# Performance work log

Measured on AMD Instinct MI355X. Metric: run time of the kernel, lower is better.

The kernel has to match this reference:

```python
import jax, jax.numpy as jnp
import numpy as np

# Module config (matches init_kwargs)
SHAPE = (96, 128, 128)   # (D, H, W)
NUM_LAYERS = 2
K, S, P, DIL = 3, 2, 1, 1  # kernel, stride, padding, dilation (dilation=1)


def _sparse_maxpool(feat, mask):
    """One SparseMaxPool3d layer on a densified sparse tensor.

    feat: [B, D, H, W, C] float, inactive sites hold dtype-min
    mask: [B, D, H, W, 1] float 0/1 activity mask
    Max is taken only over ACTIVE input sites in each window (spconv semantics);
    an output site is active iff any input in its window is active.
    """
    neg = jnp.finfo(feat.dtype).min
    window = (1, K, K, K, 1)
    strides = (1, S, S, S, 1)
    pad = [(0, 0), (P, P), (P, P), (P, P), (0, 0)]
    masked = jnp.where(mask > 0, feat, neg)
    pooled = jax.lax.reduce_window(masked, neg, jax.lax.max, window, strides, pad)
    mask_out = jax.lax.reduce_window(mask, jnp.array(0, feat.dtype).item() * 0.0,
                                     jax.lax.max, window, strides, pad)
    return pooled, mask_out


def setup_inputs() -> dict:
    key = jax.random.key(0)
    k1, k2, k3, k4, k5 = jax.random.split(key, 5)
    N, C, B = 200000, 32, 2
    D, H, W = SHAPE
    features = jax.random.normal(k1, (N, C), dtype=jnp.float32)
    b = jax.random.randint(k2, (N,), 0, B)
    z = jax.random.randint(k3, (N,), 0, D)
    y = jax.random.randint(k4, (N,), 0, H)
    x = jax.random.randint(k5, (N,), 0, W)
    coors = jnp.stack([b, z, y, x], axis=1).astype(jnp.int32)
    return {"features": features, "coors": coors, "batch_size": B}


def reference(features, coors, batch_size):
    D, H, W = SHAPE
    C = features.shape[1]
    b, z, y, x = coors[:, 0], coors[:, 1], coors[:, 2], coors[:, 3]
    neg = jnp.finfo(features.dtype).min
    # Densify the sparse tensor (duplicate coords resolved by max, inactive = -inf)
    dense = jnp.full((batch_size, D, H, W, C), neg, features.dtype)
    dense = dense.at[b, z, y, x].max(features)
    mask = jnp.zeros((batch_size, D, H, W, 1), features.dtype).at[b, z, y, x].set(1.0)
    for _ in range(NUM_LAYERS):
        dense, mask = _sparse_maxpool(dense, mask)
    # Equivalent of SparseConvTensor.dense(): inactive output sites are 0
    return jnp.where(mask > 0, dense, jnp.zeros((), features.dtype))
```

## Files before the change

### kernel.cpp

```cpp
#include <hip/hip_runtime.h>
#include <cfloat>
#include <cstdint>

#define B_    2
#define OD    24
#define OH    32
#define OW    32
#define NC    32
#define NBINS (B_ * OD * OH * OW)
#define RSTRIDE 16
#define OVF_CAP 100000

#define TZ 4
#define TY 4
#define TX 4
#define TCELLS 64
#define NTZ (OD/TZ)
#define NTY (OH/TY)
#define NTX (OW/TX)
#define NTILES (B_*NTZ*NTY*NTX)
#define NBZ (TZ+1)
#define NBY (TY+1)
#define NBX (TX+1)
#define NB  (NBZ*NBY*NBX)
#define LIST_CAP 1792

__device__ __forceinline__ unsigned xform(float f) {
    unsigned u = __float_as_uint(f);
    return u ^ ((unsigned)((int)u >> 31) | 0x80000000u);
}
__device__ __forceinline__ float unxform(unsigned t) {
    return (t == 0u) ? 0.0f
           : __uint_as_float((t >> 31) ? (t ^ 0x80000000u) : ~t);
}

__device__ __forceinline__ void slow_apply(unsigned* sm_out, const float* feat,
                                           int rec, int fm, int cb) {
    unsigned idx = ((unsigned)rec) >> 8;
    for (int c2 = 0; c2 < NC; ++c2) {
        unsigned tvv = xform(feat[idx * NC + c2]);
#pragma unroll
        for (int k = 0; k < 8; ++k) {
            const int koff = ((k & 1) * (TY * TX) + ((k >> 1) & 1) * TX
                           + ((k >> 2) & 1)) * NC;
            if ((fm >> k) & 1) atomicMax(&sm_out[cb * NC + koff + c2], tvv);
        }
    }
}


__global__ __launch_bounds__(256) void k_zero(int* __restrict__ counts,
                                              int* __restrict__ ovf_n) {
    int i = blockIdx.x * blockDim.x + threadIdx.x;
    if (i < NBINS) counts[i] = 0;
    if (i == 0) *ovf_n = 0;
}

__global__ __launch_bounds__(256) void k_bin(const int* __restrict__ coors,
                                             int* __restrict__ counts,
                                             int* __restrict__ records,
                                             int* __restrict__ ovf_n,
                                             int2* __restrict__ ovf, int N) {
    int i = blockIdx.x * blockDim.x + threadIdx.x;
    if (i >= N) return;
    int4 cc = reinterpret_cast<const int4*>(coors)[i];
    int bin = (((cc.x * OD + (cc.y >> 2)) * OH + (cc.z >> 2)) * OW + (cc.w >> 2));
    int mask = 0xFF;
    if (!(cc.y & 3)) mask &= 0x55;
    if (!(cc.z & 3)) mask &= 0x33;
    if (!(cc.w & 3)) mask &= 0x0F;
    int rec = (i << 8) | mask;
    int pos = atomicAdd(&counts[bin], 1);
    if (pos < RSTRIDE) {
        records[bin * RSTRIDE + pos] = rec;
    } else {
        int o = atomicAdd(ovf_n, 1);
        if (o < OVF_CAP) ovf[o] = make_int2(bin, rec);
    }
}

__global__ __launch_bounds__(512) void k_tile(const float* __restrict__ feat,
                                              const int* __restrict__ counts,
                                              const int* __restrict__ records,
                                              const int* __restrict__ ovf_n,
                                              const int2* __restrict__ ovf,
                                              float4* __restrict__ out4) {
    __shared__ unsigned sm_out[TCELLS * NC];
    __shared__ int2 list[LIST_CAP];
    __shared__ int sm_cursor;

    const int t   = (blockIdx.x & 7) * (NTILES / 8) + (blockIdx.x >> 3);
    const int tid = threadIdx.x;
    const int tx_ = t & (NTX - 1);
    const int ty_ = (t >> 3) & (NTY - 1);
    const int rest = t >> 6;
    const int b   = (rest >= NTZ) ? 1 : 0;
    const int tz_ = rest - b * NTZ;
    const int tz0 = tz_ * TZ, ty0 = ty_ * TY, tx0 = tx_ * TX;

    if (tid == 0) sm_cursor = 0;
    for (int v = tid; v < TCELLS * NC; v += 512) sm_out[v] = 0u;
    __syncthreads();

    if (tid < 4 * NB) {
        int bn  = tid >> 2;
        int sl  = tid & 3;
        int rz  = bn / (NBY * NBX);
        int rem = bn - rz * (NBY * NBX);
        int ry  = rem / NBX;
        int rx  = rem - ry * NBX;
        int bz = tz0 - 1 + rz, by = ty0 - 1 + ry, bx = tx0 - 1 + rx;
        if ((bz | by | bx) >= 0) {
            int bin = ((b * OD + bz) * OH + by) * OW + bx;
            int cnt = counts[bin]; if (cnt > RSTRIDE) cnt = RSTRIDE;
            int4 q = *(const int4*)(records + bin * RSTRIDE + sl * 4);
            int bi = rz - 1, bj = ry - 1, bl = rx - 1;
            int vm = 0xFF;
            if (bi < 0) vm &= 0xAA;  if (bi > TZ - 2) vm &= 0x55;
            if (bj < 0) vm &= 0xCC;  if (bj > TY - 2) vm &= 0x33;
            if (bl < 0) vm &= 0xF0;  if (bl > TX - 2) vm &= 0x0F;
            int cb = bi * (TY * TX) + bj * TX + bl;
            int rs0 = sl << 2;
            int f0 = (rs0 + 0 < cnt) ? (q.x & vm & 0xFF) : 0;
            int f1 = (rs0 + 1 < cnt) ? (q.y & vm & 0xFF) : 0;
            int f2 = (rs0 + 2 < cnt) ? (q.z & vm & 0xFF) : 0;
            int f3 = (rs0 + 3 < cnt) ? (q.w & vm & 0xFF) : 0;
            int nk = (f0 != 0) + (f1 != 0) + (f2 != 0) + (f3 != 0);
            if (nk) {
                int pos = atomicAdd(&sm_cursor, nk);
                if (f0) { if (pos < LIST_CAP) list[pos] = make_int2((q.x & ~0xFF) | f0, cb);
                          else slow_apply(sm_out, feat, q.x, f0, cb); ++pos; }
                if (f1) { if (pos < LIST_CAP) list[pos] = make_int2((q.y & ~0xFF) | f1, cb);
                          else slow_apply(sm_out, feat, q.y, f1, cb); ++pos; }
                if (f2) { if (pos < LIST_CAP) list[pos] = make_int2((q.z & ~0xFF) | f2, cb);
                          else slow_apply(sm_out, feat, q.z, f2, cb); ++pos; }
                if (f3) { if (pos < LIST_CAP) list[pos] = make_int2((q.w & ~0xFF) | f3, cb);
                          else slow_apply(sm_out, feat, q.w, f3, cb); ++pos; }
            }
        }
    }

    int on = *ovf_n;
    if (on > 0 && tid == 0) {
        if (on > OVF_CAP) on = OVF_CAP;
        for (int e = 0; e < on; ++e) {
            int2 ov = ovf[e];
            int bx = ov.x & (OW - 1);
            int by = (ov.x >> 5) & (OH - 1);
            int rest2 = ov.x >> 10;
            int bb = (rest2 >= OD) ? 1 : 0;
            int bz = rest2 - bb * OD;
            if (bb != b) continue;
            int rz = bz - (tz0 - 1), ry = by - (ty0 - 1), rx = bx - (tx0 - 1);
            if (rz < 0 || rz >= NBZ || ry < 0 || ry >= NBY || rx < 0 || rx >= NBX) continue;
            int bi = rz - 1, bj = ry - 1, bl = rx - 1;
            int vm = 0xFF;
            if (bi < 0) vm &= 0xAA;  if (bi > TZ - 2) vm &= 0x55;
            if (bj < 0) vm &= 0xCC;  if (bj > TY - 2) vm &= 0x33;
            if (bl < 0) vm &= 0xF0;  if (bl > TX - 2) vm &= 0x0F;
            int fm = ov.y & vm & 0xFF;
            if (fm) {
                int pos = atomicAdd(&sm_cursor, 1);
                if (pos < LIST_CAP)
                    list[pos] = make_int2((ov.y & ~0xFF) | fm,
                                          bi * (TY * TX) + bj * TX + bl);
            }
        }
    }
    __syncthreads();
    int total = sm_cursor; if (total > LIST_CAP) total = LIST_CAP;

    const int s = tid >> 5;
    const int c = tid & 31;

    for (int j0 = s; j0 < total; j0 += 128) {
        int2 e[8];
        unsigned tv[8];
#pragma unroll
        for (int u = 0; u < 8; ++u) {
            int j = j0 + 16 * u;
            e[u] = (j < total) ? list[j] : make_int2(0, 0);
        }
#pragma unroll
        for (int u = 0; u < 8; ++u)
            tv[u] = xform(feat[(((unsigned)e[u].x) >> 8) * NC + c]);
#pragma unroll
        for (int u = 0; u < 8; ++u) {
#pragma unroll
            for (int k = 0; k < 8; ++k) {
                const int koff = ((k & 1) * (TY * TX) + ((k >> 1) & 1) * TX
                               + ((k >> 2) & 1)) * NC + c;
                if ((e[u].x >> k) & 1) atomicMax(&sm_out[e[u].y * NC + koff], tv[u]);
            }
        }
    }
    __syncthreads();

    {
        const int cell = tid >> 3, quad = tid & 7;
        const int i = cell >> 4, jj = (cell >> 2) & 3, l = cell & 3;
        uint4 uv = *(const uint4*)&sm_out[cell * NC + quad * 4];
        float4 o;
        o.x = unxform(uv.x); o.y = unxform(uv.y);
        o.z = unxform(uv.z); o.w = unxform(uv.w);
        out4[(((size_t)(b * OD + tz0 + i) * OH + (ty0 + jj)) * OW
              + (tx0 + l)) * (NC / 4) + quad] = o;
    }
}


extern "C" void kernel_launch(void* const* d_in, const int* in_sizes, int n_in,
                              void* d_out, int out_size, void* d_ws, size_t ws_size,
                              hipStream_t stream) {
    const float* feat  = (const float*)d_in[0];
    const int*   coors = (const int*)d_in[1];
    const int N = in_sizes[0] / NC;
    float4* out4 = (float4*)d_out;

    int*  counts  = (int*)d_ws;
    int*  ovf_n   = counts + NBINS;
    int*  records = counts + NBINS + 8;
    int2* ovf     = (int2*)(records + (size_t)NBINS * RSTRIDE);

    k_zero<<<(NBINS + 255) / 256, 256, 0, stream>>>(counts, ovf_n);
    k_bin <<<(N + 255) / 256, 256, 0, stream>>>(coors, counts, records,
                                                ovf_n, ovf, N);
    k_tile<<<NTILES, 512, 0, stream>>>(feat, counts, records,
                                       ovf_n, (const int2*)ovf, out4);
}
```

Measured before the change: 41.15 us.

## Bin points directly into per-tile sublists instead of per-cell bins

The binning kernel now computes, for each input point, every output tile its pooling footprint touches, and appends a record with a precomputed footprint mask and cell offset to one of 16 sublists per tile. This removes the tile kernel's shared-memory gather stage, its shared cursor atomics and one block-wide barrier. Each 32-lane group then streams its own global sublist directly. In exchange, boundary points are duplicated into several tile lists, the binning kernel does more global atomics, and the overflow path is scanned by one group per tile.

```diff
diff --git a/kernel.cpp b/kernel.cpp
--- a/kernel.cpp
+++ b/kernel.cpp
@@ -7,9 +7,6 @@
 #define OH    32
 #define OW    32
 #define NC    32
-#define NBINS (B_ * OD * OH * OW)
-#define RSTRIDE 16
-#define OVF_CAP 100000
 
 #define TZ 4
 #define TY 4
@@ -19,11 +16,10 @@
 #define NTY (OH/TY)
 #define NTX (OW/TX)
 #define NTILES (B_*NTZ*NTY*NTX)
-#define NBZ (TZ+1)
-#define NBY (TY+1)
-#define NBX (TX+1)
-#define NB  (NBZ*NBY*NBX)
-#define LIST_CAP 1792
+#define SUBL  16
+#define SCAP  64
+#define NCUR  (NTILES*SUBL)
+#define OVF2  65536
 
 __device__ __forceinline__ unsigned xform(float f) {
     unsigned u = __float_as_uint(f);
@@ -34,60 +30,69 @@
            : __uint_as_float((t >> 31) ? (t ^ 0x80000000u) : ~t);
 }
 
-__device__ __forceinline__ void slow_apply(unsigned* sm_out, const float* feat,
-                                           int rec, int fm, int cb) {
-    unsigned idx = ((unsigned)rec) >> 8;
-    for (int c2 = 0; c2 < NC; ++c2) {
-        unsigned tvv = xform(feat[idx * NC + c2]);
-#pragma unroll
-        for (int k = 0; k < 8; ++k) {
-            const int koff = ((k & 1) * (TY * TX) + ((k >> 1) & 1) * TX
-                           + ((k >> 2) & 1)) * NC;
-            if ((fm >> k) & 1) atomicMax(&sm_out[cb * NC + koff + c2], tvv);
+
+__global__ __launch_bounds__(256) void k_zero(int* __restrict__ cursor,
+                                              int* __restrict__ ovf_n) {
+    int i = blockIdx.x * blockDim.x + threadIdx.x;
+    if (i < NCUR) cursor[i] = 0;
+    if (i == 0) *ovf_n = 0;
+}
+
+__global__ __launch_bounds__(256) void k_bin(const int* __restrict__ coors,
+                                             int* __restrict__ cursor,
+                                             int2* __restrict__ lists,
+                                             int* __restrict__ ovf_n,
+                                             int4* __restrict__ ovf, int N) {
+    int i = blockIdx.x * blockDim.x + threadIdx.x;
+    if (i >= N) return;
+    int4 cc = reinterpret_cast<const int4*>(coors)[i];
+    const int b = cc.x;
+    const int bz = cc.y >> 2, by = cc.z >> 2, bx = cc.w >> 2;
+    int mask = 0xFF;
+    if (!(cc.y & 3) || bz + 1 >= OD) mask &= 0x55;
+    if (!(cc.z & 3) || by + 1 >= OH) mask &= 0x33;
+    if (!(cc.w & 3) || bx + 1 >= OW) mask &= 0x0F;
+
+    const int tzA = bz >> 2;  const bool zB = (mask & 0xAA) && ((bz & 3) == 3);
+    const int szA = 0x55 | (((bz & 3) == 3) ? 0 : 0xAA);
+    const int tyA = by >> 2;  const bool yB = (mask & 0xCC) && ((by & 3) == 3);
+    const int syA = 0x33 | (((by & 3) == 3) ? 0 : 0xCC);
+    const int txA = bx >> 2;  const bool xB = (mask & 0xF0) && ((bx & 3) == 3);
+    const int sxA = 0x0F | (((bx & 3) == 3) ? 0 : 0xF0);
+
+    const int rec = i << 8;
+    const int sl  = i & (SUBL - 1);
+    for (int az = 0; az <= (int)zB; ++az) {
+        const int tz = tzA + az, sz = az ? 0xAA : szA;
+        for (int ay = 0; ay <= (int)yB; ++ay) {
+            const int ty = tyA + ay, sy = ay ? 0xCC : syA;
+            for (int ax = 0; ax <= (int)xB; ++ax) {
+                const int tx = txA + ax, sx = ax ? 0xF0 : sxA;
+                const int fm = mask & sz & sy & sx;
+                if (!fm) continue;
+                const int t  = ((b * NTZ + tz) * NTY + ty) * NTX + tx;
+                const int cb = (bz - tz * TZ) * (TY * TX) + (by - ty * TY) * TX
+                             + (bx - tx * TX);
+                const int sub = t * SUBL + sl;
+                int pos = atomicAdd(&cursor[sub], 1);
+                if (pos < SCAP) {
+                    lists[sub * SCAP + pos] = make_int2(rec | fm, cb);
+                } else {
+                    int o = atomicAdd(ovf_n, 1);
+                    if (o < OVF2) ovf[o] = make_int4(t, rec | fm, cb, 0);
+                }
+            }
         }
     }
 }
 
-
-__global__ __launch_bounds__(256) void k_zero(int* __restrict__ counts,
-                                              int* __restrict__ ovf_n) {
-    int i = blockIdx.x * blockDim.x + threadIdx.x;
-    if (i < NBINS) counts[i] = 0;
-    if (i == 0) *ovf_n = 0;
-}
-
-__global__ __launch_bounds__(256) void k_bin(const int* __restrict__ coors,
-                                             int* __restrict__ counts,
-                                             int* __restrict__ records,
-                                             int* __restrict__ ovf_n,
-                                             int2* __restrict__ ovf, int N) {
-    int i = blockIdx.x * blockDim.x + threadIdx.x;
-    if (i >= N) return;
-    int4 cc = reinterpret_cast<const int4*>(coors)[i];
-    int bin = (((cc.x * OD + (cc.y >> 2)) * OH + (cc.z >> 2)) * OW + (cc.w >> 2));
-    int mask = 0xFF;
-    if (!(cc.y & 3)) mask &= 0x55;
-    if (!(cc.z & 3)) mask &= 0x33;
-    if (!(cc.w & 3)) mask &= 0x0F;
-    int rec = (i << 8) | mask;
-    int pos = atomicAdd(&counts[bin], 1);
-    if (pos < RSTRIDE) {
-        records[bin * RSTRIDE + pos] = rec;
-    } else {
-        int o = atomicAdd(ovf_n, 1);
-        if (o < OVF_CAP) ovf[o] = make_int2(bin, rec);
-    }
-}
-
 __global__ __launch_bounds__(512) void k_tile(const float* __restrict__ feat,
-                                              const int* __restrict__ counts,
-                                              const int* __restrict__ records,
+                                              const int* __restrict__ cursor,
+                                              const int2* __restrict__ lists,
                                               const int* __restrict__ ovf_n,
-                                              const int2* __restrict__ ovf,
+                                              const int4* __restrict__ ovf,
                                               float4* __restrict__ out4) {
     __shared__ unsigned sm_out[TCELLS * NC];
-    __shared__ int2 list[LIST_CAP];
-    __shared__ int sm_cursor;
 
     const int t   = (blockIdx.x & 7) * (NTILES / 8) + (blockIdx.x >> 3);
     const int tid = threadIdx.x;
@@ -98,89 +103,21 @@
     const int tz_ = rest - b * NTZ;
     const int tz0 = tz_ * TZ, ty0 = ty_ * TY, tx0 = tx_ * TX;
 
-    if (tid == 0) sm_cursor = 0;
     for (int v = tid; v < TCELLS * NC; v += 512) sm_out[v] = 0u;
     __syncthreads();
 
-    if (tid < 4 * NB) {
-        int bn  = tid >> 2;
-        int sl  = tid & 3;
-        int rz  = bn / (NBY * NBX);
-        int rem = bn - rz * (NBY * NBX);
-        int ry  = rem / NBX;
-        int rx  = rem - ry * NBX;
-        int bz = tz0 - 1 + rz, by = ty0 - 1 + ry, bx = tx0 - 1 + rx;
-        if ((bz | by | bx) >= 0) {
-            int bin = ((b * OD + bz) * OH + by) * OW + bx;
-            int cnt = counts[bin]; if (cnt > RSTRIDE) cnt = RSTRIDE;
-            int4 q = *(const int4*)(records + bin * RSTRIDE + sl * 4);
-            int bi = rz - 1, bj = ry - 1, bl = rx - 1;
-            int vm = 0xFF;
-            if (bi < 0) vm &= 0xAA;  if (bi > TZ - 2) vm &= 0x55;
-            if (bj < 0) vm &= 0xCC;  if (bj > TY - 2) vm &= 0x33;
-            if (bl < 0) vm &= 0xF0;  if (bl > TX - 2) vm &= 0x0F;
-            int cb = bi * (TY * TX) + bj * TX + bl;
-            int rs0 = sl << 2;
-            int f0 = (rs0 + 0 < cnt) ? (q.x & vm & 0xFF) : 0;
-            int f1 = (rs0 + 1 < cnt) ? (q.y & vm & 0xFF) : 0;
-            int f2 = (rs0 + 2 < cnt) ? (q.z & vm & 0xFF) : 0;
-            int f3 = (rs0 + 3 < cnt) ? (q.w & vm & 0xFF) : 0;
-            int nk = (f0 != 0) + (f1 != 0) + (f2 != 0) + (f3 != 0);
-            if (nk) {
-                int pos = atomicAdd(&sm_cursor, nk);
-                if (f0) { if (pos < LIST_CAP) list[pos] = make_int2((q.x & ~0xFF) | f0, cb);
-                          else slow_apply(sm_out, feat, q.x, f0, cb); ++pos; }
-                if (f1) { if (pos < LIST_CAP) list[pos] = make_int2((q.y & ~0xFF) | f1, cb);
-                          else slow_apply(sm_out, feat, q.y, f1, cb); ++pos; }
-                if (f2) { if (pos < LIST_CAP) list[pos] = make_int2((q.z & ~0xFF) | f2, cb);
-                          else slow_apply(sm_out, feat, q.z, f2, cb); ++pos; }
-                if (f3) { if (pos < LIST_CAP) list[pos] = make_int2((q.w & ~0xFF) | f3, cb);
-                          else slow_apply(sm_out, feat, q.w, f3, cb); ++pos; }
-            }
-        }
-    }
-
-    int on = *ovf_n;
-    if (on > 0 && tid == 0) {
-        if (on > OVF_CAP) on = OVF_CAP;
-        for (int e = 0; e < on; ++e) {
-            int2 ov = ovf[e];
-            int bx = ov.x & (OW - 1);
-            int by = (ov.x >> 5) & (OH - 1);
-            int rest2 = ov.x >> 10;
-            int bb = (rest2 >= OD) ? 1 : 0;
-            int bz = rest2 - bb * OD;
-            if (bb != b) continue;
-            int rz = bz - (tz0 - 1), ry = by - (ty0 - 1), rx = bx - (tx0 - 1);
-            if (rz < 0 || rz >= NBZ || ry < 0 || ry >= NBY || rx < 0 || rx >= NBX) continue;
-            int bi = rz - 1, bj = ry - 1, bl = rx - 1;
-            int vm = 0xFF;
-            if (bi < 0) vm &= 0xAA;  if (bi > TZ - 2) vm &= 0x55;
-            if (bj < 0) vm &= 0xCC;  if (bj > TY - 2) vm &= 0x33;
-            if (bl < 0) vm &= 0xF0;  if (bl > TX - 2) vm &= 0x0F;
-            int fm = ov.y & vm & 0xFF;
-            if (fm) {
-                int pos = atomicAdd(&sm_cursor, 1);
-                if (pos < LIST_CAP)
-                    list[pos] = make_int2((ov.y & ~0xFF) | fm,
-                                          bi * (TY * TX) + bj * TX + bl);
-            }
-        }
-    }
-    __syncthreads();
-    int total = sm_cursor; if (total > LIST_CAP) total = LIST_CAP;
-
     const int s = tid >> 5;
     const int c = tid & 31;
+    const int sub = t * SUBL + s;
+    int cnt = cursor[sub]; if (cnt > SCAP) cnt = SCAP;
+    const int2* L = lists + (size_t)sub * SCAP;
 
-    for (int j0 = s; j0 < total; j0 += 128) {
+    for (int j0 = 0; j0 < cnt; j0 += 8) {
         int2 e[8];
         unsigned tv[8];
 #pragma unroll
-        for (int u = 0; u < 8; ++u) {
-            int j = j0 + 16 * u;
-            e[u] = (j < total) ? list[j] : make_int2(0, 0);
-        }
+        for (int u = 0; u < 8; ++u)
+            e[u] = (j0 + u < cnt) ? L[j0 + u] : make_int2(0, 0);
 #pragma unroll
         for (int u = 0; u < 8; ++u)
             tv[u] = xform(feat[(((unsigned)e[u].x) >> 8) * NC + c]);
@@ -188,9 +125,28 @@
         for (int u = 0; u < 8; ++u) {
 #pragma unroll
             for (int k = 0; k < 8; ++k) {
-                const int koff = ((k & 1) * (TY * TX) + ((k >> 1) & 1) * TX
-                               + ((k >> 2) & 1)) * NC + c;
-                if ((e[u].x >> k) & 1) atomicMax(&sm_out[e[u].y * NC + koff], tv[u]);
+                const int koff = (k & 1) * (TY * TX) + ((k >> 1) & 1) * TX
+                               + ((k >> 2) & 1);
+                if ((e[u].x >> k) & 1)
+                    atomicMax(&sm_out[(e[u].y + koff) * NC + c], tv[u]);
+            }
+        }
+    }
+
+    int on = *ovf_n;
+    if (on > 0 && s == 0) {
+        if (on > OVF2) on = OVF2;
+        for (int j = 0; j < on; ++j) {
+            int4 e = ovf[j];
+            if (e.x != t) continue;
+            unsigned tvv = xform(feat[(((unsigned)e.y) >> 8) * NC + c]);
+            const int fm = e.y & 0xFF, cb = e.z;
+#pragma unroll
+            for (int k = 0; k < 8; ++k) {
+                const int koff = (k & 1) * (TY * TX) + ((k >> 1) & 1) * TX
+                               + ((k >> 2) & 1);
+                if ((fm >> k) & 1)
+                    atomicMax(&sm_out[(cb + koff) * NC + c], tvv);
             }
         }
     }
@@ -217,14 +173,14 @@
     const int N = in_sizes[0] / NC;
     float4* out4 = (float4*)d_out;
 
-    int*  counts  = (int*)d_ws;
-    int*  ovf_n   = counts + NBINS;
-    int*  records = counts + NBINS + 8;
-    int2* ovf     = (int2*)(records + (size_t)NBINS * RSTRIDE);
+    int*  cursor = (int*)d_ws;
+    int*  ovf_n  = cursor + NCUR;
+    int2* lists  = (int2*)(ovf_n + 8);
+    int4* ovf    = (int4*)(lists + (size_t)NTILES * SUBL * SCAP);
 
-    k_zero<<<(NBINS + 255) / 256, 256, 0, stream>>>(counts, ovf_n);
-    k_bin <<<(N + 255) / 256, 256, 0, stream>>>(coors, counts, records,
+    k_zero<<<(NCUR + 255) / 256, 256, 0, stream>>>(cursor, ovf_n);
+    k_bin <<<(N + 255) / 256, 256, 0, stream>>>(coors, cursor, lists,
                                                 ovf_n, ovf, N);
-    k_tile<<<NTILES, 512, 0, stream>>>(feat, counts, records,
-                                       ovf_n, (const int2*)ovf, out4);
+    k_tile<<<NTILES, 512, 0, stream>>>(feat, cursor, (const int2*)lists,
+                                       ovf_n, (const int4*)ovf, out4);
 }
```

Measured after the change: 54.81 us. 1.33x slower.

## Reduce each bin in registers before LDS atomics, dropping the shared work list

Applied to the files above, without the earlier changes.

Replaces the two-phase scheme, which built a shared-memory list of records and then scattered per-record atomics, with a per-bin loop. One 32-lane group (one lane per channel) walks every record of a bin and keeps 8 register maxima, one per output cell the bin feeds. Then it issues one LDS atomicMax per touched cell. This removes the list build, a barrier and most of the LDS atomic traffic. In exchange, the feature loads within a bin are serialized per group and the per-group load is less even, since 125 bins are spread across 16 groups.

```diff
diff --git a/kernel.cpp b/kernel.cpp
--- a/kernel.cpp
+++ b/kernel.cpp
@@ -19,11 +19,7 @@
 #define NTY (OH/TY)
 #define NTX (OW/TX)
 #define NTILES (B_*NTZ*NTY*NTX)
-#define NBZ (TZ+1)
-#define NBY (TY+1)
-#define NBX (TX+1)
-#define NB  (NBZ*NBY*NBX)
-#define LIST_CAP 1792
+#define NB  125
 
 __device__ __forceinline__ unsigned xform(float f) {
     unsigned u = __float_as_uint(f);
@@ -86,8 +82,6 @@
                                               const int2* __restrict__ ovf,
                                               float4* __restrict__ out4) {
     __shared__ unsigned sm_out[TCELLS * NC];
-    __shared__ int2 list[LIST_CAP];
-    __shared__ int sm_cursor;
 
     const int t   = (blockIdx.x & 7) * (NTILES / 8) + (blockIdx.x >> 3);
     const int tid = threadIdx.x;
@@ -98,47 +92,70 @@
     const int tz_ = rest - b * NTZ;
     const int tz0 = tz_ * TZ, ty0 = ty_ * TY, tx0 = tx_ * TX;
 
-    if (tid == 0) sm_cursor = 0;
     for (int v = tid; v < TCELLS * NC; v += 512) sm_out[v] = 0u;
     __syncthreads();
 
-    if (tid < 4 * NB) {
-        int bn  = tid >> 2;
-        int sl  = tid & 3;
-        int rz  = bn / (NBY * NBX);
-        int rem = bn - rz * (NBY * NBX);
-        int ry  = rem / NBX;
-        int rx  = rem - ry * NBX;
+    const int s  = tid >> 5;
+    const int ch = tid & 31;
+
+#define PROC(R, RS) do {                                                     \
+    if ((RS) < cnt) {                                                        \
+        int fm = (R) & vm & 0xFF;                                            \
+        if (fm) {                                                            \
+            float f = feat[(((unsigned)(R)) >> 8) * NC + ch];                \
+            kb |= fm;                                                        \
+            _Pragma("unroll")                                                \
+            for (int k = 0; k < 8; ++k)                                      \
+                if ((fm >> k) & 1) m[k] = fmaxf(m[k], f);                    \
+        }                                                                    \
+    } } while (0)
+
+    for (int pass = 0; pass < 8; ++pass) {
+        int bn = pass * 16 + s;
+        if (bn >= NB) break;
+        int rz  = bn / 25;
+        int rem = bn - rz * 25;
+        int ry  = rem / 5;
+        int rx  = rem - ry * 5;
         int bz = tz0 - 1 + rz, by = ty0 - 1 + ry, bx = tx0 - 1 + rx;
-        if ((bz | by | bx) >= 0) {
-            int bin = ((b * OD + bz) * OH + by) * OW + bx;
-            int cnt = counts[bin]; if (cnt > RSTRIDE) cnt = RSTRIDE;
-            int4 q = *(const int4*)(records + bin * RSTRIDE + sl * 4);
-            int bi = rz - 1, bj = ry - 1, bl = rx - 1;
-            int vm = 0xFF;
-            if (bi < 0) vm &= 0xAA;  if (bi > TZ - 2) vm &= 0x55;
-            if (bj < 0) vm &= 0xCC;  if (bj > TY - 2) vm &= 0x33;
-            if (bl < 0) vm &= 0xF0;  if (bl > TX - 2) vm &= 0x0F;
-            int cb = bi * (TY * TX) + bj * TX + bl;
-            int rs0 = sl << 2;
-            int f0 = (rs0 + 0 < cnt) ? (q.x & vm & 0xFF) : 0;
-            int f1 = (rs0 + 1 < cnt) ? (q.y & vm & 0xFF) : 0;
-            int f2 = (rs0 + 2 < cnt) ? (q.z & vm & 0xFF) : 0;
-            int f3 = (rs0 + 3 < cnt) ? (q.w & vm & 0xFF) : 0;
-            int nk = (f0 != 0) + (f1 != 0) + (f2 != 0) + (f3 != 0);
-            if (nk) {
-                int pos = atomicAdd(&sm_cursor, nk);
-                if (f0) { if (pos < LIST_CAP) list[pos] = make_int2((q.x & ~0xFF) | f0, cb);
-                          else slow_apply(sm_out, feat, q.x, f0, cb); ++pos; }
-                if (f1) { if (pos < LIST_CAP) list[pos] = make_int2((q.y & ~0xFF) | f1, cb);
-                          else slow_apply(sm_out, feat, q.y, f1, cb); ++pos; }
-                if (f2) { if (pos < LIST_CAP) list[pos] = make_int2((q.z & ~0xFF) | f2, cb);
-                          else slow_apply(sm_out, feat, q.z, f2, cb); ++pos; }
-                if (f3) { if (pos < LIST_CAP) list[pos] = make_int2((q.w & ~0xFF) | f3, cb);
-                          else slow_apply(sm_out, feat, q.w, f3, cb); ++pos; }
+        if ((bz | by | bx) < 0) continue;
+        int bin = ((b * OD + bz) * OH + by) * OW + bx;
+        int cnt = counts[bin]; if (cnt > RSTRIDE) cnt = RSTRIDE;
+        if (cnt == 0) continue;
+        int bi = rz - 1, bj = ry - 1, bl = rx - 1;
+        int vm = 0xFF;
+        if (bi < 0) vm &= 0xAA;  if (bi > TZ - 2) vm &= 0x55;
+        if (bj < 0) vm &= 0xCC;  if (bj > TY - 2) vm &= 0x33;
+        if (bl < 0) vm &= 0xF0;  if (bl > TX - 2) vm &= 0x0F;
+        if (!vm) continue;
+        int cb = bi * (TY * TX) + bj * TX + bl;
+
+        float m[8];
+#pragma unroll
+        for (int k = 0; k < 8; ++k) m[k] = -FLT_MAX;
+        int kb = 0;
+        const int4* rp = (const int4*)(records + bin * RSTRIDE);
+#pragma unroll
+        for (int g = 0; g < 4; ++g) {
+            if (g * 4 >= cnt) break;
+            int4 q = rp[g];
+            PROC(q.x, g * 4 + 0);
+            PROC(q.y, g * 4 + 1);
+            PROC(q.z, g * 4 + 2);
+            PROC(q.w, g * 4 + 3);
+        }
+        if (kb) {
+#pragma unroll
+            for (int k = 0; k < 8; ++k) {
+                if ((kb >> k) & 1) {
+                    const int koff = (k & 1) * (TY * TX) + ((k >> 1) & 1) * TX
+                                   + ((k >> 2) & 1);
+                    atomicMax(&sm_out[(cb + koff) * NC + ch], xform(m[k]));
+                }
             }
         }
     }
+#undef PROC
 
     int on = *ovf_n;
     if (on > 0 && tid == 0) {
@@ -152,46 +169,15 @@
             int bz = rest2 - bb * OD;
             if (bb != b) continue;
             int rz = bz - (tz0 - 1), ry = by - (ty0 - 1), rx = bx - (tx0 - 1);
-            if (rz < 0 || rz >= NBZ || ry < 0 || ry >= NBY || rx < 0 || rx >= NBX) continue;
+            if (rz < 0 || rz >= 5 || ry < 0 || ry >= 5 || rx < 0 || rx >= 5) continue;
             int bi = rz - 1, bj = ry - 1, bl = rx - 1;
             int vm = 0xFF;
             if (bi < 0) vm &= 0xAA;  if (bi > TZ - 2) vm &= 0x55;
             if (bj < 0) vm &= 0xCC;  if (bj > TY - 2) vm &= 0x33;
             if (bl < 0) vm &= 0xF0;  if (bl > TX - 2) vm &= 0x0F;
             int fm = ov.y & vm & 0xFF;
-            if (fm) {
-                int pos = atomicAdd(&sm_cursor, 1);
-                if (pos < LIST_CAP)
-                    list[pos] = make_int2((ov.y & ~0xFF) | fm,
-                                          bi * (TY * TX) + bj * TX + bl);
-            }
-        }
-    }
-    __syncthreads();
-    int total = sm_cursor; if (total > LIST_CAP) total = LIST_CAP;
-
-    const int s = tid >> 5;
-    const int c = tid & 31;
-
-    for (int j0 = s; j0 < total; j0 += 128) {
-        int2 e[8];
-        unsigned tv[8];
-#pragma unroll
-        for (int u = 0; u < 8; ++u) {
-            int j = j0 + 16 * u;
-            e[u] = (j < total) ? list[j] : make_int2(0, 0);
-        }
-#pragma unroll
-        for (int u = 0; u < 8; ++u)
-            tv[u] = xform(feat[(((unsigned)e[u].x) >> 8) * NC + c]);
-#pragma unroll
-        for (int u = 0; u < 8; ++u) {
-#pragma unroll
-            for (int k = 0; k < 8; ++k) {
-                const int koff = ((k & 1) * (TY * TX) + ((k >> 1) & 1) * TX
-                               + ((k >> 2) & 1)) * NC + c;
-                if ((e[u].x >> k) & 1) atomicMax(&sm_out[e[u].y * NC + koff], tv[u]);
-            }
+            if (fm) slow_apply(sm_out, feat, ov.y, fm,
+                               bi * (TY * TX) + bj * TX + bl);
         }
     }
     __syncthreads();
```

After: 58.83 us. 1.43x slower.
